# Kernel tuning notes

Hardware: AMD Instinct MI355X
Metric: run time of the kernel (lower is better)

Reference implementation:

```python
import jax, jax.numpy as jnp
import numpy as np

N0 = 292864   # input (hop-2) nodes
N1 = 11264    # hop-1 nodes
B = 1024      # target nodes
F_IN, HID, OUT = 128, 256, 47
E0, E1 = 281600, 10240
H_HIT = 146432
N_CACHE, N_GLOBAL, C_FEAT = 50000, 100000, 200000
P = 2048


def setup_inputs() -> dict:
    key = jax.random.key(0)
    ks = jax.random.split(key, 20)
    perm = jax.random.permutation(ks[0], N0)
    hit_pos = perm[:H_HIT]
    miss_pos = perm[H_HIT:]
    x = jax.random.normal(ks[1], (N0 - H_HIT, F_IN), jnp.float32)
    feat_cache = jax.random.normal(ks[2], (C_FEAT, F_IN), jnp.float32)
    hit_idx = jax.random.randint(ks[3], (H_HIT,), 0, C_FEAT)
    edge_index0 = jnp.stack([jax.random.randint(ks[4], (E0,), 0, N0),
                             jax.random.randint(ks[5], (E0,), 0, N1)])
    edge_index1 = jnp.stack([jax.random.randint(ks[6], (E1,), 0, N1),
                             jax.random.randint(ks[7], (E1,), 0, B)])
    emb_cache = jax.random.normal(ks[8], (N_CACHE, HID), jnp.float32)
    emb_cache_table = jax.random.randint(ks[9], (N_GLOBAL,), 0, N_CACHE)
    push_batch_id = jax.random.randint(ks[10], (P,), 0, N1)
    push_global_id = jax.random.randint(ks[11], (P,), 0, N_GLOBAL)
    pull_batch_id = jax.random.randint(ks[12], (P,), 0, N1)
    pull_global_id = jax.random.randint(ks[13], (P,), 0, N_GLOBAL)
    W0_l = jax.random.normal(ks[14], (F_IN, HID), jnp.float32) / np.sqrt(F_IN)
    b0_l = jnp.zeros((HID,), jnp.float32)
    W0_r = jax.random.normal(ks[15], (F_IN, HID), jnp.float32) / np.sqrt(F_IN)
    W1_l = jax.random.normal(ks[16], (HID, OUT), jnp.float32) / np.sqrt(HID)
    b1_l = jnp.zeros((OUT,), jnp.float32)
    W1_r = jax.random.normal(ks[17], (HID, OUT), jnp.float32) / np.sqrt(HID)
    return dict(x=x, feat_cache=feat_cache, emb_cache=emb_cache, hit_idx=hit_idx,
                hit_pos=hit_pos, miss_pos=miss_pos, edge_index0=edge_index0,
                edge_index1=edge_index1, emb_cache_table=emb_cache_table,
                push_batch_id=push_batch_id, push_global_id=push_global_id,
                pull_batch_id=pull_batch_id, pull_global_id=pull_global_id,
                W0_l=W0_l, b0_l=b0_l, W0_r=W0_r, W1_l=W1_l, b1_l=b1_l, W1_r=W1_r)


def _sage_conv(h_src, h_dst, edge_index, n_dst, W_l, b_l, W_r):
    # PyG SAGEConv (mean aggr): out = lin_l(mean_j x_j) + lin_r(x_i)
    src, dst = edge_index[0], edge_index[1]
    msg = h_src[src]                                              # [E, F] gather
    s = jax.ops.segment_sum(msg, dst, num_segments=n_dst)        # scatter-add
    cnt = jax.ops.segment_sum(jnp.ones((src.shape[0],), h_src.dtype), dst,
                              num_segments=n_dst)[:, None]
    mean = s / jnp.maximum(cnt, 1.0)
    return mean @ W_l + b_l + h_dst @ W_r


def reference(x, feat_cache, emb_cache, hit_idx, hit_pos, miss_pos,
              edge_index0, edge_index1, emb_cache_table,
              push_batch_id, push_global_id, pull_batch_id, pull_global_id,
              W0_l, b0_l, W0_r, W1_l, b1_l, W1_r):
    # Assemble node features from pinned feature cache (hits) + fetched feats (misses)
    h = jnp.zeros((N0, F_IN), x.dtype)
    h = h.at[hit_pos].set(feat_cache[hit_idx]).at[miss_pos].set(x)
    # Layer 0 (inner hop)
    h = _sage_conv(h, h[:N1], edge_index0, N1, W0_l, b0_l, W0_r)
    h = jax.nn.relu(h)  # dropout p=0.5 skipped (eval mode)
    # Last layer: push stale embeddings into cache, then pull cached embeddings
    slots_push = emb_cache_table[push_global_id]
    emb_cache = emb_cache.at[slots_push].set(jax.lax.stop_gradient(h[push_batch_id]))
    pulled = jax.lax.stop_gradient(emb_cache[emb_cache_table[pull_global_id]])
    h = h.at[pull_batch_id].set(pulled)
    out = _sage_conv(h, h[:B], edge_index1, B, W1_l, b1_l, W1_r)
    return jax.nn.log_softmax(out, axis=-1)
```

## Files before the change

kernel.cpp:

```cpp
#include <hip/hip_runtime.h>
#include <math.h>

#define N0c     292864
#define N1c     11264
#define Bc      1024
#define F_INc   128
#define HIDc    256
#define OUTc    47
#define E0c     281600
#define E1c     10240
#define H_HITc  146432
#define N_CACHEc 50000
#define C_FEATc 200000
#define Pc      2048

__global__ void prep_kernel(const int* __restrict__ hit_pos, const int* __restrict__ hit_idx,
                            const int* __restrict__ miss_pos, int* __restrict__ map,
                            int* __restrict__ cur0, int* __restrict__ pwin,
                            int* __restrict__ cur1, int* __restrict__ win,
                            int* __restrict__ src_row) {
  int i = blockIdx.x * 256 + threadIdx.x;
  if (i < H_HITc) {
    map[hit_pos[i]]  = hit_idx[i];
    map[miss_pos[i]] = C_FEATc + i;
  }
  if (i < N1c) { cur0[i] = 0; pwin[i] = -1; src_row[i] = i; }
  if (i < Bc)  cur1[i] = 0;
  if (i < N_CACHEc) win[i] = -1;
}

__global__ void deg_both_kernel(const int* __restrict__ e0, const int* __restrict__ e1,
                                int* __restrict__ deg0, int* __restrict__ deg1) {
  int i = blockIdx.x * 256 + threadIdx.x;
  if (i < E0c) {
    atomicAdd(&deg0[e0[E0c + i]], 1);
  } else if (i < E0c + E1c) {
    int j = i - E0c;
    atomicAdd(&deg1[e1[E1c + j]], 1);
  }
}

__device__ void scan_block(const int* __restrict__ deg, int* __restrict__ off,
                           int* __restrict__ cur, int n) {
  __shared__ int wsum[16];
  int tid = threadIdx.x;
  int lane = tid & 63, wid = tid >> 6;
  int ITEMS = (n + 1023) >> 10;
  int base = tid * ITEMS;
  int v[12];
  int sum = 0;
  for (int j = 0; j < ITEMS; ++j) {
    int i = base + j;
    v[j] = (i < n) ? deg[i] : 0;
    sum += v[j];
  }
  int s = sum;
  for (int o = 1; o < 64; o <<= 1) {
    int t = __shfl_up(s, o);
    if (lane >= o) s += t;
  }
  if (lane == 63) wsum[wid] = s;
  __syncthreads();
  if (tid < 16) {
    int w = wsum[tid];
    for (int o = 1; o < 16; o <<= 1) {
      int t = __shfl_up(w, o);
      if (tid >= o) w += t;
    }
    wsum[tid] = w;
  }
  __syncthreads();
  int wbase = (wid > 0) ? wsum[wid - 1] : 0;
  int run = wbase + s - sum;
  for (int j = 0; j < ITEMS; ++j) {
    int i = base + j;
    if (i < n) { off[i] = run; cur[i] = run; run += v[j]; }
  }
  if (tid == 1023) off[n] = run;
}

__global__ __launch_bounds__(1024) void scan_both_kernel(
    int* __restrict__ cur0, int* __restrict__ off0,
    int* __restrict__ cur1, int* __restrict__ off1) {
  if (blockIdx.x == 0) scan_block(cur0, off0, cur0, N1c);
  else                 scan_block(cur1, off1, cur1, Bc);
}

__global__ void scatter_both_kernel(const int* __restrict__ e0, const int* __restrict__ e1,
                                    const int* __restrict__ map,
                                    int* __restrict__ cur0, int* __restrict__ esrc0,
                                    int* __restrict__ cur1, int* __restrict__ esrc1) {
  int i = blockIdx.x * 256 + threadIdx.x;
  if (i < E0c) {
    int p = atomicAdd(&cur0[e0[E0c + i]], 1);
    esrc0[p] = map[e0[i]];
  } else if (i < E0c + E1c) {
    int j = i - E0c;
    int p = atomicAdd(&cur1[e1[E1c + j]], 1);
    esrc1[p] = e1[j];
  }
}

__global__ __launch_bounds__(256) void agg1_kernel(
    const int* __restrict__ off, const int* __restrict__ esrc,
    const float* __restrict__ fc, const float* __restrict__ x,
    float4* __restrict__ mean4) {
  __shared__ float4 sbuf[8][32];
  int d = blockIdx.x;
  int slot = threadIdx.x >> 5, lane = threadIdx.x & 31;
  int s = off[d], e = off[d + 1];
  float4 acc0 = make_float4(0.f, 0.f, 0.f, 0.f);
  float4 acc1 = make_float4(0.f, 0.f, 0.f, 0.f);
  int i0 = s + slot, i1 = s + slot + 8;
  int m0 = (i0 < e) ? esrc[i0] : -1;
  int m1 = (i1 < e) ? esrc[i1] : -1;
  while (i0 < e) {
    int i0n = i0 + 16, i1n = i1 + 16;
    int m0n = (i0n < e) ? esrc[i0n] : -1;
    int m1n = (i1n < e) ? esrc[i1n] : -1;
    const float* r0 = (m0 < C_FEATc) ? (fc + (size_t)m0 * F_INc)
                                     : (x + (size_t)(m0 - C_FEATc) * F_INc);
    float4 v0 = ((const float4*)r0)[lane];
    if (i1 < e) {
      const float* r1 = (m1 < C_FEATc) ? (fc + (size_t)m1 * F_INc)
                                       : (x + (size_t)(m1 - C_FEATc) * F_INc);
      float4 v1 = ((const float4*)r1)[lane];
      acc1.x += v1.x; acc1.y += v1.y; acc1.z += v1.z; acc1.w += v1.w;
    }
    acc0.x += v0.x; acc0.y += v0.y; acc0.z += v0.z; acc0.w += v0.w;
    i0 = i0n; m0 = m0n; i1 = i1n; m1 = m1n;
  }
  acc0.x += acc1.x; acc0.y += acc1.y; acc0.z += acc1.z; acc0.w += acc1.w;
  sbuf[slot][lane] = acc0;
  __syncthreads();
  if (slot < 4) {
    float4 o = sbuf[slot + 4][lane];
    acc0.x += o.x; acc0.y += o.y; acc0.z += o.z; acc0.w += o.w;
    sbuf[slot][lane] = acc0;
  }
  __syncthreads();
  if (slot < 2) {
    float4 o = sbuf[slot + 2][lane];
    acc0.x += o.x; acc0.y += o.y; acc0.z += o.z; acc0.w += o.w;
    sbuf[slot][lane] = acc0;
  }
  __syncthreads();
  if (slot == 0) {
    float4 o = sbuf[1][lane];
    acc0.x += o.x; acc0.y += o.y; acc0.z += o.z; acc0.w += o.w;
    float inv = 1.f / fmaxf((float)(e - s), 1.f);
    mean4[(size_t)d * 32 + lane] = make_float4(acc0.x * inv, acc0.y * inv,
                                               acc0.z * inv, acc0.w * inv);
  }
}

#define ROWS1 16
__global__ __launch_bounds__(256) void gemm1_kernel(
    const float4* __restrict__ mean4, const int* __restrict__ map,
    const float* __restrict__ fc, const float* __restrict__ x,
    const float* __restrict__ W0l, const float* __restrict__ b0,
    const float* __restrict__ W0r, float* __restrict__ h1) {
  __shared__ float lin[ROWS1][256];
  int g0 = blockIdx.x * ROWS1;
  int tid = threadIdx.x;
  for (int idx = tid; idx < ROWS1 * 32; idx += 256) {
    int r = idx >> 5, l = idx & 31;
    ((float4*)&lin[r][0])[l] = mean4[(size_t)(g0 + r) * 32 + l];
  }
  for (int idx = tid; idx < ROWS1 * 32; idx += 256) {
    int r = idx >> 5, l = idx & 31;
    int m = map[g0 + r];
    const float* row = (m < C_FEATc) ? (fc + (size_t)m * F_INc)
                                     : (x + (size_t)(m - C_FEATc) * F_INc);
    ((float4*)&lin[r][128])[l] = ((const float4*)row)[l];
  }
  __syncthreads();
  int col = tid;
  float acc[ROWS1];
#pragma unroll
  for (int r = 0; r < ROWS1; ++r) acc[r] = 0.f;
  for (int kb = 0; kb < 32; ++kb) {
    float w0 = W0l[(kb * 4 + 0) * 256 + col];
    float w1 = W0l[(kb * 4 + 1) * 256 + col];
    float w2 = W0l[(kb * 4 + 2) * 256 + col];
    float w3 = W0l[(kb * 4 + 3) * 256 + col];
#pragma unroll
    for (int r = 0; r < ROWS1; ++r) {
      float4 a = *(const float4*)&lin[r][kb * 4];
      acc[r] += a.x * w0 + a.y * w1 + a.z * w2 + a.w * w3;
    }
  }
  for (int kb = 0; kb < 32; ++kb) {
    float w0 = W0r[(kb * 4 + 0) * 256 + col];
    float w1 = W0r[(kb * 4 + 1) * 256 + col];
    float w2 = W0r[(kb * 4 + 2) * 256 + col];
    float w3 = W0r[(kb * 4 + 3) * 256 + col];
#pragma unroll
    for (int r = 0; r < ROWS1; ++r) {
      float4 a = *(const float4*)&lin[r][128 + kb * 4];
      acc[r] += a.x * w0 + a.y * w1 + a.z * w2 + a.w * w3;
    }
  }
  float b = b0[col];
#pragma unroll
  for (int r = 0; r < ROWS1; ++r) {
    float v = acc[r] + b;
    h1[(size_t)(g0 + r) * HIDc + col] = v > 0.f ? v : 0.f;
  }
}

__global__ void win_both_kernel(const int* __restrict__ push_gid, const int* __restrict__ table,
                                int* __restrict__ win,
                                const int* __restrict__ pull_bid, int* __restrict__ pwin) {
  int i = blockIdx.x * 256 + threadIdx.x;
  if (i < Pc) atomicMax(&win[table[push_gid[i]]], i);
  else if (i < 2 * Pc) {
    int j = i - Pc;
    atomicMax(&pwin[pull_bid[j]], j);
  }
}

__global__ void resolve_kernel(const int* __restrict__ pull_bid, const int* __restrict__ pull_gid,
                               const int* __restrict__ table, const int* __restrict__ win,
                               const int* __restrict__ pwin, const int* __restrict__ push_bid,
                               int* __restrict__ src_row) {
  int i = blockIdx.x * 256 + threadIdx.x;
  if (i >= Pc) return;
  int b = pull_bid[i];
  if (pwin[b] != i) return;
  int slot = table[pull_gid[i]];
  int j = win[slot];
  src_row[b] = (j >= 0) ? push_bid[j] : (N1c + slot);
}

__global__ __launch_bounds__(256) void conv2_kernel(
    const int* __restrict__ off, const int* __restrict__ esrc,
    const int* __restrict__ src_row,
    const float* __restrict__ h1, const float* __restrict__ emb,
    const float* __restrict__ W1l, const float* __restrict__ b1,
    const float* __restrict__ W1r, float* __restrict__ out) {
  __shared__ float lin[512];
  __shared__ float partial[64][4];
  int row = blockIdx.x;
  int t = threadIdx.x;
  int s = off[row], e = off[row + 1];
  float acc = 0.f;
  for (int i = s; i < e; ++i) {
    int m = src_row[esrc[i]];
    const float* rp = (m < N1c) ? (h1 + (size_t)m * HIDc)
                                : (emb + (size_t)(m - N1c) * HIDc);
    acc += rp[t];
  }
  lin[t] = acc / fmaxf((float)(e - s), 1.f);
  {
    int m = src_row[row];
    const float* rp = (m < N1c) ? (h1 + (size_t)m * HIDc)
                                : (emb + (size_t)(m - N1c) * HIDc);
    lin[256 + t] = rp[t];
  }
  __syncthreads();
  int col = t >> 2;
  int seg = t & 3;
  float p = 0.f;
  if (col < OUTc) {
    int k0 = seg * 64;
    for (int k = k0; k < k0 + 64; ++k) p += lin[k] * W1l[k * OUTc + col];
    for (int k = k0; k < k0 + 64; ++k) p += lin[256 + k] * W1r[k * OUTc + col];
  }
  partial[col][seg] = p;
  __syncthreads();
  if (t < 64) {
    float v = partial[t][0] + partial[t][1] + partial[t][2] + partial[t][3];
    if (t < OUTc) v += b1[t];
    float vv = (t < OUTc) ? v : -INFINITY;
    float m = vv;
    for (int o = 32; o > 0; o >>= 1) m = fmaxf(m, __shfl_xor(m, o));
    float ex = (t < OUTc) ? expf(vv - m) : 0.f;
    float sum = ex;
    for (int o = 32; o > 0; o >>= 1) sum += __shfl_xor(sum, o);
    if (t < OUTc) out[(size_t)row * OUTc + t] = vv - m - logf(sum);
  }
}

extern "C" void kernel_launch(void* const* d_in, const int* in_sizes, int n_in,
                              void* d_out, int out_size, void* d_ws, size_t ws_size,
                              hipStream_t stream) {
  const float* x          = (const float*)d_in[0];
  const float* feat_cache = (const float*)d_in[1];
  const float* emb_cache  = (const float*)d_in[2];
  const int* hit_idx      = (const int*)d_in[3];
  const int* hit_pos      = (const int*)d_in[4];
  const int* miss_pos     = (const int*)d_in[5];
  const int* e0           = (const int*)d_in[6];
  const int* e1           = (const int*)d_in[7];
  const int* table        = (const int*)d_in[8];
  const int* push_bid     = (const int*)d_in[9];
  const int* push_gid     = (const int*)d_in[10];
  const int* pull_bid     = (const int*)d_in[11];
  const int* pull_gid     = (const int*)d_in[12];
  const float* W0l        = (const float*)d_in[13];
  const float* b0         = (const float*)d_in[14];
  const float* W0r        = (const float*)d_in[15];
  const float* W1l        = (const float*)d_in[16];
  const float* b1         = (const float*)d_in[17];
  const float* W1r        = (const float*)d_in[18];
  float* out = (float*)d_out;

  char* p = (char*)d_ws;
  size_t ob = 0;
  auto take = [&](size_t bytes) -> void* {
    void* r = p + ob;
    ob += (bytes + 255) & ~(size_t)255;
    return r;
  };
  int* MAP     = (int*)take((size_t)N0c * 4);
  int* OFF0    = (int*)take((size_t)(N1c + 1) * 4);
  int* CUR0    = (int*)take((size_t)N1c * 4);
  int* ESRC0   = (int*)take((size_t)E0c * 4);
  float* MEAN1 = (float*)take((size_t)N1c * F_INc * 4);
  float* H1    = (float*)take((size_t)N1c * HIDc * 4);
  int* WIN     = (int*)take((size_t)N_CACHEc * 4);
  int* PWIN    = (int*)take((size_t)N1c * 4);
  int* SRCROW  = (int*)take((size_t)N1c * 4);
  int* OFF1    = (int*)take((size_t)(Bc + 1) * 4);
  int* CUR1    = (int*)take((size_t)Bc * 4);
  int* ESRC1   = (int*)take((size_t)E1c * 4);

  prep_kernel<<<(H_HITc + 255) / 256, 256, 0, stream>>>(hit_pos, hit_idx, miss_pos,
                                                        MAP, CUR0, PWIN, CUR1, WIN, SRCROW);
  deg_both_kernel<<<(E0c + E1c + 255) / 256, 256, 0, stream>>>(e0, e1, CUR0, CUR1);
  scan_both_kernel<<<2, 1024, 0, stream>>>(CUR0, OFF0, CUR1, OFF1);
  scatter_both_kernel<<<(E0c + E1c + 255) / 256, 256, 0, stream>>>(e0, e1, MAP,
                                                                  CUR0, ESRC0, CUR1, ESRC1);
  agg1_kernel<<<N1c, 256, 0, stream>>>(OFF0, ESRC0, feat_cache, x, (float4*)MEAN1);
  gemm1_kernel<<<N1c / ROWS1, 256, 0, stream>>>((const float4*)MEAN1, MAP, feat_cache, x,
                                                W0l, b0, W0r, H1);
  win_both_kernel<<<(2 * Pc + 255) / 256, 256, 0, stream>>>(push_gid, table, WIN, pull_bid, PWIN);
  resolve_kernel<<<(Pc + 255) / 256, 256, 0, stream>>>(pull_bid, pull_gid, table, WIN,
                                                       PWIN, push_bid, SRCROW);
  conv2_kernel<<<Bc, 256, 0, stream>>>(OFF1, ESRC1, SRCROW, H1, emb_cache, W1l, b1, W1r, out);
}
```

Before: 353.9 us.

## Fold push/pull winner resolution into edge kernels and widen agg1 gather unroll

The push/pull cache-winner atomics are merged into the degree-count kernel, and the pull resolution is merged into the edge scatter kernel. This drops two separate small launches from the stream. Resolution only depends on WIN and PWIN, which are complete after the atomics kernel, so the ordering stays correct. The agg1 gather now keeps four independent accumulators with 32-edge strides per slot instead of two, giving more memory loads in flight per thread at the cost of extra registers.

Result: no change. 350.4 us (-1.0%).

```diff
diff --git a/kernel.cpp b/kernel.cpp
--- a/kernel.cpp
+++ b/kernel.cpp
@@ -29,14 +29,23 @@
   if (i < N_CACHEc) win[i] = -1;
 }
 
-__global__ void deg_both_kernel(const int* __restrict__ e0, const int* __restrict__ e1,
-                                int* __restrict__ deg0, int* __restrict__ deg1) {
+__global__ void atomics_kernel(const int* __restrict__ e0, const int* __restrict__ e1,
+                               int* __restrict__ deg0, int* __restrict__ deg1,
+                               const int* __restrict__ push_gid, const int* __restrict__ table,
+                               int* __restrict__ win,
+                               const int* __restrict__ pull_bid, int* __restrict__ pwin) {
   int i = blockIdx.x * 256 + threadIdx.x;
   if (i < E0c) {
     atomicAdd(&deg0[e0[E0c + i]], 1);
   } else if (i < E0c + E1c) {
     int j = i - E0c;
     atomicAdd(&deg1[e1[E1c + j]], 1);
+  } else if (i < E0c + E1c + Pc) {
+    int j = i - E0c - E1c;
+    atomicMax(&win[table[push_gid[j]]], j);
+  } else if (i < E0c + E1c + 2 * Pc) {
+    int j = i - E0c - E1c - Pc;
+    atomicMax(&pwin[pull_bid[j]], j);
   }
 }
 
@@ -86,10 +95,14 @@
   else                 scan_block(cur1, off1, cur1, Bc);
 }
 
-__global__ void scatter_both_kernel(const int* __restrict__ e0, const int* __restrict__ e1,
-                                    const int* __restrict__ map,
-                                    int* __restrict__ cur0, int* __restrict__ esrc0,
-                                    int* __restrict__ cur1, int* __restrict__ esrc1) {
+__global__ void scatter_resolve_kernel(const int* __restrict__ e0, const int* __restrict__ e1,
+                                       const int* __restrict__ map,
+                                       int* __restrict__ cur0, int* __restrict__ esrc0,
+                                       int* __restrict__ cur1, int* __restrict__ esrc1,
+                                       const int* __restrict__ pull_bid, const int* __restrict__ pull_gid,
+                                       const int* __restrict__ table, const int* __restrict__ win,
+                                       const int* __restrict__ pwin, const int* __restrict__ push_bid,
+                                       int* __restrict__ src_row) {
   int i = blockIdx.x * 256 + threadIdx.x;
   if (i < E0c) {
     int p = atomicAdd(&cur0[e0[E0c + i]], 1);
@@ -98,6 +111,14 @@
     int j = i - E0c;
     int p = atomicAdd(&cur1[e1[E1c + j]], 1);
     esrc1[p] = e1[j];
+  } else if (i < E0c + E1c + Pc) {
+    int j = i - E0c - E1c;
+    int b = pull_bid[j];
+    if (pwin[b] == j) {
+      int slot = table[pull_gid[j]];
+      int w = win[slot];
+      src_row[b] = (w >= 0) ? push_bid[w] : (N1c + slot);
+    }
   }
 }
 
@@ -109,48 +130,69 @@
   int d = blockIdx.x;
   int slot = threadIdx.x >> 5, lane = threadIdx.x & 31;
   int s = off[d], e = off[d + 1];
-  float4 acc0 = make_float4(0.f, 0.f, 0.f, 0.f);
-  float4 acc1 = make_float4(0.f, 0.f, 0.f, 0.f);
-  int i0 = s + slot, i1 = s + slot + 8;
+  float4 a0 = make_float4(0.f, 0.f, 0.f, 0.f);
+  float4 a1 = a0, a2 = a0, a3 = a0;
+  int i0 = s + slot, i1 = i0 + 8, i2 = i0 + 16, i3 = i0 + 24;
   int m0 = (i0 < e) ? esrc[i0] : -1;
   int m1 = (i1 < e) ? esrc[i1] : -1;
+  int m2 = (i2 < e) ? esrc[i2] : -1;
+  int m3 = (i3 < e) ? esrc[i3] : -1;
   while (i0 < e) {
-    int i0n = i0 + 16, i1n = i1 + 16;
-    int m0n = (i0n < e) ? esrc[i0n] : -1;
-    int m1n = (i1n < e) ? esrc[i1n] : -1;
-    const float* r0 = (m0 < C_FEATc) ? (fc + (size_t)m0 * F_INc)
-                                     : (x + (size_t)(m0 - C_FEATc) * F_INc);
-    float4 v0 = ((const float4*)r0)[lane];
+    int n0 = i0 + 32, n1 = i1 + 32, n2 = i2 + 32, n3 = i3 + 32;
+    int p0 = (n0 < e) ? esrc[n0] : -1;
+    int p1 = (n1 < e) ? esrc[n1] : -1;
+    int p2 = (n2 < e) ? esrc[n2] : -1;
+    int p3 = (n3 < e) ? esrc[n3] : -1;
+    {
+      const float* r = (m0 < C_FEATc) ? (fc + (size_t)m0 * F_INc)
+                                      : (x + (size_t)(m0 - C_FEATc) * F_INc);
+      float4 v = ((const float4*)r)[lane];
+      a0.x += v.x; a0.y += v.y; a0.z += v.z; a0.w += v.w;
+    }
     if (i1 < e) {
-      const float* r1 = (m1 < C_FEATc) ? (fc + (size_t)m1 * F_INc)
-                                       : (x + (size_t)(m1 - C_FEATc) * F_INc);
-      float4 v1 = ((const float4*)r1)[lane];
-      acc1.x += v1.x; acc1.y += v1.y; acc1.z += v1.z; acc1.w += v1.w;
-    }
-    acc0.x += v0.x; acc0.y += v0.y; acc0.z += v0.z; acc0.w += v0.w;
-    i0 = i0n; m0 = m0n; i1 = i1n; m1 = m1n;
-  }
-  acc0.x += acc1.x; acc0.y += acc1.y; acc0.z += acc1.z; acc0.w += acc1.w;
-  sbuf[slot][lane] = acc0;
+      const float* r = (m1 < C_FEATc) ? (fc + (size_t)m1 * F_INc)
+                                      : (x + (size_t)(m1 - C_FEATc) * F_INc);
+      float4 v = ((const float4*)r)[lane];
+      a1.x += v.x; a1.y += v.y; a1.z += v.z; a1.w += v.w;
+    }
+    if (i2 < e) {
+      const float* r = (m2 < C_FEATc) ? (fc + (size_t)m2 * F_INc)
+                                      : (x + (size_t)(m2 - C_FEATc) * F_INc);
+      float4 v = ((const float4*)r)[lane];
+      a2.x += v.x; a2.y += v.y; a2.z += v.z; a2.w += v.w;
+    }
+    if (i3 < e) {
+      const float* r = (m3 < C_FEATc) ? (fc + (size_t)m3 * F_INc)
+                                      : (x + (size_t)(m3 - C_FEATc) * F_INc);
+      float4 v = ((const float4*)r)[lane];
+      a3.x += v.x; a3.y += v.y; a3.z += v.z; a3.w += v.w;
+    }
+    i0 = n0; m0 = p0; i1 = n1; m1 = p1; i2 = n2; m2 = p2; i3 = n3; m3 = p3;
+  }
+  a0.x += a1.x + a2.x + a3.x;
+  a0.y += a1.y + a2.y + a3.y;
+  a0.z += a1.z + a2.z + a3.z;
+  a0.w += a1.w + a2.w + a3.w;
+  sbuf[slot][lane] = a0;
   __syncthreads();
   if (slot < 4) {
     float4 o = sbuf[slot + 4][lane];
-    acc0.x += o.x; acc0.y += o.y; acc0.z += o.z; acc0.w += o.w;
-    sbuf[slot][lane] = acc0;
+    a0.x += o.x; a0.y += o.y; a0.z += o.z; a0.w += o.w;
+    sbuf[slot][lane] = a0;
   }
   __syncthreads();
   if (slot < 2) {
     float4 o = sbuf[slot + 2][lane];
-    acc0.x += o.x; acc0.y += o.y; acc0.z += o.z; acc0.w += o.w;
-    sbuf[slot][lane] = acc0;
+    a0.x += o.x; a0.y += o.y; a0.z += o.z; a0.w += o.w;
+    sbuf[slot][lane] = a0;
   }
   __syncthreads();
   if (slot == 0) {
     float4 o = sbuf[1][lane];
-    acc0.x += o.x; acc0.y += o.y; acc0.z += o.z; acc0.w += o.w;
+    a0.x += o.x; a0.y += o.y; a0.z += o.z; a0.w += o.w;
     float inv = 1.f / fmaxf((float)(e - s), 1.f);
-    mean4[(size_t)d * 32 + lane] = make_float4(acc0.x * inv, acc0.y * inv,
-                                               acc0.z * inv, acc0.w * inv);
+    mean4[(size_t)d * 32 + lane] = make_float4(a0.x * inv, a0.y * inv,
+                                               a0.z * inv, a0.w * inv);
   }
 }
 
@@ -207,30 +249,6 @@
     float v = acc[r] + b;
     h1[(size_t)(g0 + r) * HIDc + col] = v > 0.f ? v : 0.f;
   }
-}
-
-__global__ void win_both_kernel(const int* __restrict__ push_gid, const int* __restrict__ table,
-                                int* __restrict__ win,
-                                const int* __restrict__ pull_bid, int* __restrict__ pwin) {
-  int i = blockIdx.x * 256 + threadIdx.x;
-  if (i < Pc) atomicMax(&win[table[push_gid[i]]], i);
-  else if (i < 2 * Pc) {
-    int j = i - Pc;
-    atomicMax(&pwin[pull_bid[j]], j);
-  }
-}
-
-__global__ void resolve_kernel(const int* __restrict__ pull_bid, const int* __restrict__ pull_gid,
-                               const int* __restrict__ table, const int* __restrict__ win,
-                               const int* __restrict__ pwin, const int* __restrict__ push_bid,
-                               int* __restrict__ src_row) {
-  int i = blockIdx.x * 256 + threadIdx.x;
-  if (i >= Pc) return;
-  int b = pull_bid[i];
-  if (pwin[b] != i) return;
-  int slot = table[pull_gid[i]];
-  int j = win[slot];
-  src_row[b] = (j >= 0) ? push_bid[j] : (N1c + slot);
 }
 
 __global__ __launch_bounds__(256) void conv2_kernel(
@@ -328,15 +346,14 @@
 
   prep_kernel<<<(H_HITc + 255) / 256, 256, 0, stream>>>(hit_pos, hit_idx, miss_pos,
                                                         MAP, CUR0, PWIN, CUR1, WIN, SRCROW);
-  deg_both_kernel<<<(E0c + E1c + 255) / 256, 256, 0, stream>>>(e0, e1, CUR0, CUR1);
+  atomics_kernel<<<(E0c + E1c + 2 * Pc + 255) / 256, 256, 0, stream>>>(
+      e0, e1, CUR0, CUR1, push_gid, table, WIN, pull_bid, PWIN);
   scan_both_kernel<<<2, 1024, 0, stream>>>(CUR0, OFF0, CUR1, OFF1);
-  scatter_both_kernel<<<(E0c + E1c + 255) / 256, 256, 0, stream>>>(e0, e1, MAP,
-                                                                  CUR0, ESRC0, CUR1, ESRC1);
+  scatter_resolve_kernel<<<(E0c + E1c + Pc + 255) / 256, 256, 0, stream>>>(
+      e0, e1, MAP, CUR0, ESRC0, CUR1, ESRC1,
+      pull_bid, pull_gid, table, WIN, PWIN, push_bid, SRCROW);
   agg1_kernel<<<N1c, 256, 0, stream>>>(OFF0, ESRC0, feat_cache, x, (float4*)MEAN1);
   gemm1_kernel<<<N1c / ROWS1, 256, 0, stream>>>((const float4*)MEAN1, MAP, feat_cache, x,
                                                 W0l, b0, W0r, H1);
-  win_both_kernel<<<(2 * Pc + 255) / 256, 256, 0, stream>>>(push_gid, table, WIN, pull_bid, PWIN);
-  resolve_kernel<<<(Pc + 255) / 256, 256, 0, stream>>>(pull_bid, pull_gid, table, WIN,
-                                                       PWIN, push_bid, SRCROW);
   conv2_kernel<<<Bc, 256, 0, stream>>>(OFF1, ESRC1, SRCROW, H1, emb_cache, W1l, b1, W1r, out);
 }
```
